# Kernel tuning notes

Measured on AMD Instinct MI355X. Metric: run time of the kernel, lower is better.

## Reference

```python
import jax, jax.numpy as jnp
import numpy as np

N = 50000        # nodes
E = 100000       # directed edges
F_NODE = 22      # atom features
F_EDGE = 4       # bond features
H = 64           # hidden_dim
EPS = 1e-5       # BatchNorm eps


def setup_inputs() -> dict:
    key = jax.random.key(0)
    ks = jax.random.split(key, 16)
    s = 0.05
    return {
        "x": jax.random.normal(ks[0], (N, F_NODE), dtype=jnp.float32),
        "edge_attr": jax.random.normal(ks[1], (E, F_EDGE), dtype=jnp.float32),
        "We1": jax.random.normal(ks[2], (F_EDGE, F_NODE * H), dtype=jnp.float32) * s,
        "be1": jnp.zeros((F_NODE * H,), dtype=jnp.float32),
        "root1": jax.random.normal(ks[3], (F_NODE, H), dtype=jnp.float32) * s,
        "b1": jnp.zeros((H,), dtype=jnp.float32),
        "g1": jnp.ones((H,), dtype=jnp.float32),
        "beta1": jnp.zeros((H,), dtype=jnp.float32),
        "We2": jax.random.normal(ks[4], (F_EDGE, H * H), dtype=jnp.float32) * s,
        "be2": jnp.zeros((H * H,), dtype=jnp.float32),
        "root2": jax.random.normal(ks[5], (H, H), dtype=jnp.float32) * s,
        "b2": jnp.zeros((H,), dtype=jnp.float32),
        "g2": jnp.ones((H,), dtype=jnp.float32),
        "beta2": jnp.zeros((H,), dtype=jnp.float32),
        "Wfc": jax.random.normal(ks[6], (H, 1), dtype=jnp.float32) * s,
        "bfc": jnp.zeros((1,), dtype=jnp.float32),
        "edge_index": jax.random.randint(ks[7], (2, E), 0, N, dtype=jnp.int32),
    }


def nnconv(x, edge_index, edge_attr, We, be, root, bias, in_ch, out_ch):
    # PyG NNConv (aggr='add', root_weight=True):
    #   out_i = x_i @ root + bias + sum_{(j->i)} x_j @ reshape(MLP(e_ji), [in, out])
    src, dst = edge_index[0], edge_index[1]
    w = jax.nn.relu(edge_attr @ We + be).reshape(-1, in_ch, out_ch)  # [E, in, out]
    msg = jnp.einsum('ei,eio->eo', x[src], w)                        # [E, out]
    agg = jax.ops.segment_sum(msg, dst, num_segments=x.shape[0])     # [N, out]
    return agg + x @ root + bias


def batchnorm(x, gamma, beta):
    # training-mode BatchNorm1d: batch statistics, biased variance
    mu = jnp.mean(x, axis=0)
    var = jnp.mean(jnp.square(x - mu), axis=0)
    return (x - mu) * jax.lax.rsqrt(var + EPS) * gamma + beta


def reference(x, edge_attr, We1, be1, root1, b1, g1, beta1,
              We2, be2, root2, b2, g2, beta2, Wfc, bfc, edge_index):
    h = nnconv(x, edge_index, edge_attr, We1, be1, root1, b1, F_NODE, H)
    h = jax.nn.relu(batchnorm(h, g1, beta1))
    # dropout is identity in eval / deterministic reference
    h = nnconv(h, edge_index, edge_attr, We2, be2, root2, b2, H, H)
    h = jax.nn.relu(batchnorm(h, g2, beta2))
    return jax.nn.sigmoid(h @ Wfc + bfc)  # [N, 1]
```

## Files before the change

### kernel.cpp

```cpp
#include <hip/hip_runtime.h>
#include <math.h>

#define N_NODES 50000
#define N_EDGES 100000
#define FNODE 22
#define HDIM 64
#define BN_EPS 1e-5f

typedef __attribute__((ext_vector_type(8))) short bfrag;
typedef __attribute__((ext_vector_type(4))) float facc;
typedef __attribute__((ext_vector_type(4))) unsigned int uint4v;

__device__ __forceinline__ unsigned f2bf(float x) {
    unsigned u = __float_as_uint(x);
    return (u + 0x7FFFu + ((u >> 16) & 1u)) >> 16;
}
__device__ __forceinline__ unsigned pk2bf(float lo, float hi) {
    return f2bf(lo) | (f2bf(hi) << 16);
}

template <int K>
__global__ void k_packB(const float* __restrict__ W, uint4v* __restrict__ Bt) {
    constexpr int NQ = (K + 31) / 32;
    int t = threadIdx.x;
    int ot = t >> 6, lane = t & 63;
    int o = ot * 16 + (lane & 15);
    int kg = lane >> 4;
#pragma unroll
    for (int q = 0; q < NQ; ++q) {
        unsigned w[4];
#pragma unroll
        for (int p = 0; p < 4; ++p) {
            int k0 = q * 32 + kg * 8 + 2 * p;
            float lo = (k0 < K) ? W[k0 * HDIM + o] : 0.f;
            float hi = (k0 + 1 < K) ? W[(k0 + 1) * HDIM + o] : 0.f;
            w[p] = pk2bf(lo, hi);
        }
        Bt[(ot * NQ + q) * 64 + lane] = uint4v{w[0], w[1], w[2], w[3]};
    }
}

__global__ void k_node1(const float* __restrict__ x, const uint4v* __restrict__ Bt1,
                        const float* __restrict__ b1, float* __restrict__ h1) {
    int lane = threadIdx.x & 63;
    int m = lane & 15, kg = lane >> 4, orow4 = kg * 4;
    int tile = blockIdx.x * 4 + (threadIdx.x >> 6);
    int nb = tile * 16;
    if (nb >= N_NODES) return;
    const float* xr = x + (size_t)(nb + m) * FNODE;
    float xv[8];
#pragma unroll
    for (int p = 0; p < 4; ++p) {
        int c = kg * 8 + 2 * p;
        float2 v = (c + 1 < FNODE) ? *(const float2*)(xr + c) : float2{0.f, 0.f};
        xv[2 * p] = v.x; xv[2 * p + 1] = v.y;
    }
    bfrag A = __builtin_bit_cast(bfrag, uint4v{pk2bf(xv[0], xv[1]), pk2bf(xv[2], xv[3]),
                                               pk2bf(xv[4], xv[5]), pk2bf(xv[6], xv[7])});
    const facc zero4 = {0.f, 0.f, 0.f, 0.f};
#pragma unroll
    for (int ot = 0; ot < 4; ++ot) {
        bfrag B = __builtin_bit_cast(bfrag, Bt1[ot * 64 + lane]);
        facc d = __builtin_amdgcn_mfma_f32_16x16x32_bf16(A, B, zero4, 0, 0, 0);
        float bv = b1[ot * 16 + m];
#pragma unroll
        for (int j = 0; j < 4; ++j)
            h1[(size_t)(nb + orow4 + j) * HDIM + ot * 16 + m] = d[j] + bv;
    }
}

template <int IN, int CHUNK>
__launch_bounds__(256, 6)
__global__ void k_edge(const float* __restrict__ h, const float* __restrict__ ea,
                       const float* __restrict__ We, const float* __restrict__ be,
                       const int* __restrict__ eidx, float* __restrict__ out) {
    constexpr int INH = IN * HDIM;
    constexpr int IP = IN / 2;
    __shared__ uint4v Wd[IP * 32];
    __shared__ unsigned Bp[IP * 32];

    int obeg = (blockIdx.x & 1) * 32;
    int tileblk = blockIdx.x >> 1;

    for (int idx = threadIdx.x; idx < IP * 32; idx += 256) {
        int ip = idx >> 5, oloc = idx & 31;
        int c0 = (2 * ip) * HDIM + obeg + oloc;
        int c1 = c0 + HDIM;
        Wd[idx] = uint4v{pk2bf(We[c0], We[INH + c0]),
                         pk2bf(We[2 * INH + c0], We[3 * INH + c0]),
                         pk2bf(We[c1], We[INH + c1]),
                         pk2bf(We[2 * INH + c1], We[3 * INH + c1])};
        Bp[idx] = pk2bf(be[c0], be[c1]);
    }
    __syncthreads();

    int lane = threadIdx.x & 63;
    int e16 = lane & 15;
    int orow4 = (lane >> 4) * 4;
    int tile = tileblk * 4 + (threadIdx.x >> 6);
    int ebase = tile * 16;
    if (ebase >= N_EDGES) return;

    bool act = lane < 16;
    float4 ea0 = ((const float4*)ea)[ebase + e16];
    bfrag A0 = __builtin_bit_cast(bfrag, uint4v{act ? pk2bf(ea0.x, ea0.y) : 0u,
                                                act ? pk2bf(ea0.z, ea0.w) : 0u, 0u, 0u});

    const char* hb = (const char*)h;
    unsigned offA[4];
#pragma unroll
    for (int j = 0; j < 4; ++j)
        offA[j] = (unsigned)eidx[ebase + orow4 + j] * (IN * 4);

    const facc zero4 = {0.f, 0.f, 0.f, 0.f};
    facc m0[2] = {zero4, zero4};

#pragma unroll
    for (int i0 = 0; i0 < IN; i0 += CHUNK) {
        float cA[4][CHUNK];
#pragma unroll
        for (int j = 0; j < 4; ++j) {
            if constexpr (CHUNK == 4) {
                float4 v = *(const float4*)(hb + offA[j] + (size_t)i0 * 4);
                cA[j][0] = v.x; cA[j][1] = v.y; cA[j][2] = v.z; cA[j][3] = v.w;
            } else {
                float2 v = *(const float2*)(hb + offA[j] + (size_t)i0 * 4);
                cA[j][0] = v.x; cA[j][1] = v.y;
            }
        }
#pragma unroll
        for (int t = 0; t < 2; ++t) {
#pragma unroll
            for (int d2 = 0; d2 < CHUNK / 2; ++d2) {
                int ip = i0 / 2 + d2;
                uint4v wq = Wd[ip * 32 + t * 16 + e16];
                unsigned bq = Bp[ip * 32 + t * 16 + e16];
                float bl = __uint_as_float(bq << 16);
                float bh = __uint_as_float(bq & 0xFFFF0000u);
                facc cl = {bl, bl, bl, bl};
                facc ch = {bh, bh, bh, bh};
                bfrag Blo = __builtin_bit_cast(bfrag, uint4v{wq.x, wq.y, 0u, 0u});
                bfrag Bhi = __builtin_bit_cast(bfrag, uint4v{wq.z, wq.w, 0u, 0u});
                facc t0 = __builtin_amdgcn_mfma_f32_16x16x32_bf16(A0, Blo, cl, 0, 0, 0);
#pragma unroll
                for (int j = 0; j < 4; ++j)
                    m0[t][j] = fmaf(cA[j][2 * d2], fmaxf(t0[j], 0.f), m0[t][j]);
                t0 = __builtin_amdgcn_mfma_f32_16x16x32_bf16(A0, Bhi, ch, 0, 0, 0);
#pragma unroll
                for (int j = 0; j < 4; ++j)
                    m0[t][j] = fmaf(cA[j][2 * d2 + 1], fmaxf(t0[j], 0.f), m0[t][j]);
            }
        }
    }

    int dA[4];
#pragma unroll
    for (int j = 0; j < 4; ++j)
        dA[j] = eidx[N_EDGES + ebase + orow4 + j];
#pragma unroll
    for (int t = 0; t < 2; ++t) {
#pragma unroll
        for (int j = 0; j < 4; ++j)
            atomicAdd(&out[(size_t)dA[j] * HDIM + obeg + t * 16 + e16], m0[t][j]);
    }
}

__global__ void k_stats(const float* __restrict__ hbuf, float* stats) {
    int c = threadIdx.x & 63;
    int r = threadIdx.x >> 6;
    int rowsPer = blockDim.x >> 6;
    float s = 0.f, q = 0.f;
    for (int n = blockIdx.x * rowsPer + r; n < N_NODES; n += gridDim.x * rowsPer) {
        float v = hbuf[n * HDIM + c];
        s += v;
        q = fmaf(v, v, q);
    }
    __shared__ float ls[4][64], lq[4][64];
    ls[r][c] = s;
    lq[r][c] = q;
    __syncthreads();
    if (r == 0) {
        s = ls[0][c] + ls[1][c] + ls[2][c] + ls[3][c];
        q = lq[0][c] + lq[1][c] + lq[2][c] + lq[3][c];
        atomicAdd(&stats[c], s);
        atomicAdd(&stats[64 + c], q);
    }
}

__global__ void k_finalize(const float* stats_in, const float* __restrict__ g,
                           const float* __restrict__ beta, float* as_out) {
    int c = threadIdx.x;
    float mu = stats_in[c] * (1.f / N_NODES);
    float var = stats_in[64 + c] * (1.f / N_NODES) - mu * mu;
    var = fmaxf(var, 0.f);
    float a = g[c] * rsqrtf(var + BN_EPS);
    as_out[c] = a;
    as_out[64 + c] = beta[c] - mu * a;
}

__global__ void k_apply1(const float* h1, const float* __restrict__ as1,
                         const uint4v* __restrict__ Bt, const float* __restrict__ b2,
                         float* __restrict__ h1n, float* h2) {
    int lane = threadIdx.x & 63;
    int m = lane & 15, kg = lane >> 4, orow4 = (lane >> 4) * 4;
    int tile = blockIdx.x * 4 + (threadIdx.x >> 6);
    int nb = tile * 16;
    if (nb >= N_NODES) return;
    int node = nb + m;
    const float* hr = h1 + (size_t)node * HDIM;

    float4 a0 = *(const float4*)(as1 + kg * 8), a1 = *(const float4*)(as1 + kg * 8 + 4);
    float4 s0 = *(const float4*)(as1 + 64 + kg * 8), s1 = *(const float4*)(as1 + 64 + kg * 8 + 4);
    float4 a2 = *(const float4*)(as1 + 32 + kg * 8), a3 = *(const float4*)(as1 + 32 + kg * 8 + 4);
    float4 s2 = *(const float4*)(as1 + 96 + kg * 8), s3 = *(const float4*)(as1 + 96 + kg * 8 + 4);

    float4 v0 = *(const float4*)(hr + kg * 8), v1 = *(const float4*)(hr + kg * 8 + 4);
    float4 v2 = *(const float4*)(hr + 32 + kg * 8), v3 = *(const float4*)(hr + 32 + kg * 8 + 4);

    float r0[8], r1[8];
#pragma unroll
    for (int p = 0; p < 4; ++p) {
        r0[p]     = fmaxf(fmaf((&v0.x)[p], (&a0.x)[p], (&s0.x)[p]), 0.f);
        r0[p + 4] = fmaxf(fmaf((&v1.x)[p], (&a1.x)[p], (&s1.x)[p]), 0.f);
        r1[p]     = fmaxf(fmaf((&v2.x)[p], (&a2.x)[p], (&s2.x)[p]), 0.f);
        r1[p + 4] = fmaxf(fmaf((&v3.x)[p], (&a3.x)[p], (&s3.x)[p]), 0.f);
    }
    *(float4*)(h1n + (size_t)node * HDIM + kg * 8)     = float4{r0[0], r0[1], r0[2], r0[3]};
    *(float4*)(h1n + (size_t)node * HDIM + kg * 8 + 4) = float4{r0[4], r0[5], r0[6], r0[7]};
    *(float4*)(h1n + (size_t)node * HDIM + 32 + kg * 8)     = float4{r1[0], r1[1], r1[2], r1[3]};
    *(float4*)(h1n + (size_t)node * HDIM + 32 + kg * 8 + 4) = float4{r1[4], r1[5], r1[6], r1[7]};

    bfrag A0 = __builtin_bit_cast(bfrag, uint4v{pk2bf(r0[0], r0[1]), pk2bf(r0[2], r0[3]),
                                                pk2bf(r0[4], r0[5]), pk2bf(r0[6], r0[7])});
    bfrag A1 = __builtin_bit_cast(bfrag, uint4v{pk2bf(r1[0], r1[1]), pk2bf(r1[2], r1[3]),
                                                pk2bf(r1[4], r1[5]), pk2bf(r1[6], r1[7])});

    const facc zero4 = {0.f, 0.f, 0.f, 0.f};
#pragma unroll
    for (int ot = 0; ot < 4; ++ot) {
        bfrag B0 = __builtin_bit_cast(bfrag, Bt[(ot * 2 + 0) * 64 + lane]);
        bfrag B1 = __builtin_bit_cast(bfrag, Bt[(ot * 2 + 1) * 64 + lane]);
        facc d = __builtin_amdgcn_mfma_f32_16x16x32_bf16(A0, B0, zero4, 0, 0, 0);
        d = __builtin_amdgcn_mfma_f32_16x16x32_bf16(A1, B1, d, 0, 0, 0);
        float bv = b2[ot * 16 + m];
#pragma unroll
        for (int j = 0; j < 4; ++j)
            h2[(size_t)(nb + orow4 + j) * HDIM + ot * 16 + m] = d[j] + bv;
    }
}

__global__ void k_final(const float* __restrict__ h2, const float* __restrict__ as2,
                        const float* __restrict__ Wfc, const float* __restrict__ bfc,
                        float* __restrict__ out) {
    int lane = threadIdx.x & 63;
    int n = blockIdx.x * (blockDim.x >> 6) + (threadIdx.x >> 6);
    if (n >= N_NODES) return;
    float a = as2[lane], s = as2[64 + lane];
    float v = fmaxf(fmaf(h2[n * HDIM + lane], a, s), 0.f) * Wfc[lane];
#pragma unroll
    for (int off = 32; off > 0; off >>= 1) v += __shfl_xor(v, off, 64);
    if (lane == 0) out[n] = 1.f / (1.f + expf(-(v + bfc[0])));
}

extern "C" void kernel_launch(void* const* d_in, const int* in_sizes, int n_in,
                              void* d_out, int out_size, void* d_ws, size_t ws_size,
                              hipStream_t stream) {
    const float* x     = (const float*)d_in[0];
    const float* ea    = (const float*)d_in[1];
    const float* We1   = (const float*)d_in[2];
    const float* be1   = (const float*)d_in[3];
    const float* root1 = (const float*)d_in[4];
    const float* b1    = (const float*)d_in[5];
    const float* g1    = (const float*)d_in[6];
    const float* beta1 = (const float*)d_in[7];
    const float* We2   = (const float*)d_in[8];
    const float* be2   = (const float*)d_in[9];
    const float* root2 = (const float*)d_in[10];
    const float* b2    = (const float*)d_in[11];
    const float* g2    = (const float*)d_in[12];
    const float* beta2 = (const float*)d_in[13];
    const float* Wfc   = (const float*)d_in[14];
    const float* bfc   = (const float*)d_in[15];
    const int*   eidx  = (const int*)d_in[16];
    float* out = (float*)d_out;

    char* ws = (char*)d_ws;
    const size_t nbuf = (size_t)N_NODES * HDIM * sizeof(float);
    float* h1    = (float*)ws;
    float* h1n   = (float*)(ws + nbuf);
    float* h2    = h1;
    float* stats = (float*)(ws + 2 * nbuf);
    uint4v* Bt2  = (uint4v*)(ws + 2 * nbuf + 4096);
    uint4v* Bt1  = (uint4v*)(ws + 2 * nbuf + 4096 + 8192);

    hipMemsetAsync(stats, 0, 512 * sizeof(float), stream);
    k_packB<HDIM><<<1, 256, 0, stream>>>(root2, Bt2);
    k_packB<FNODE><<<1, 256, 0, stream>>>(root1, Bt1);

    const int edgeBlocks = 2 * ((N_EDGES / 16 + 3) / 4);
    const int nodeBlocks = (N_NODES + 3) / 4;
    const int tileBlocks = (N_NODES / 16 + 3) / 4;

    k_node1<<<tileBlocks, 256, 0, stream>>>(x, Bt1, b1, h1);
    k_edge<FNODE, 2><<<edgeBlocks, 256, 0, stream>>>(x, ea, We1, be1, eidx, h1);
    k_stats<<<256, 256, 0, stream>>>(h1, stats);
    k_finalize<<<1, 64, 0, stream>>>(stats, g1, beta1, stats + 128);
    k_apply1<<<tileBlocks, 256, 0, stream>>>(h1, stats + 128, Bt2, b2, h1n, h2);
    k_edge<HDIM, 4><<<edgeBlocks, 256, 0, stream>>>(h1n, ea, We2, be2, eidx, h2);
    k_stats<<<256, 256, 0, stream>>>(h2, stats + 256);
    k_finalize<<<1, 64, 0, stream>>>(stats + 256, g2, beta2, stats + 384);
    k_final<<<nodeBlocks, 256, 0, stream>>>(h2, stats + 384, Wfc, bfc, out);
}
```

Before: 172.8 us.

## Replace atomic scatter-add with CSR-based gather reduction of per-edge messages

Builds a CSR index of edges grouped by destination node each call (count, scan, scatter kernels). Edge kernels now write per-edge messages to a buffer instead of doing float atomicAdds into node rows, and a new reduce kernel sums each node's incoming messages. This removes atomic contention. In exchange it adds a 25.6MB message buffer write and read per layer, plus several extra launches, including a single-block scan.

New measurement: 312.3 us. 80.8% more time.

```diff
diff --git a/kernel.cpp b/kernel.cpp
--- a/kernel.cpp
+++ b/kernel.cpp
@@ -17,6 +17,60 @@
 }
 __device__ __forceinline__ unsigned pk2bf(float lo, float hi) {
     return f2bf(lo) | (f2bf(hi) << 16);
+}
+
+__global__ void k_count(const int* __restrict__ eidx, int* __restrict__ cnt) {
+    int e = blockIdx.x * 256 + threadIdx.x;
+    if (e < N_EDGES) atomicAdd(&cnt[eidx[N_EDGES + e]], 1);
+}
+
+__global__ void k_scan(const int* __restrict__ cnt, int* __restrict__ base,
+                       int* __restrict__ cursor) {
+    __shared__ int part[1024];
+    int t = threadIdx.x;
+    const int PER = (N_NODES + 1023) / 1024;
+    int beg = t * PER;
+    int end = min(beg + PER, N_NODES);
+    int s = 0;
+    for (int i = beg; i < end; ++i) s += cnt[i];
+    part[t] = s;
+    __syncthreads();
+    for (int off = 1; off < 1024; off <<= 1) {
+        int v = part[t];
+        int u = (t >= off) ? part[t - off] : 0;
+        __syncthreads();
+        part[t] = v + u;
+        __syncthreads();
+    }
+    int run = (t == 0) ? 0 : part[t - 1];
+    for (int i = beg; i < end; ++i) {
+        base[i] = run;
+        cursor[i] = run;
+        run += cnt[i];
+    }
+    if (t == 1023) base[N_NODES] = part[1023];
+}
+
+__global__ void k_scatter(const int* __restrict__ eidx, int* __restrict__ cursor,
+                          int* __restrict__ csr) {
+    int e = blockIdx.x * 256 + threadIdx.x;
+    if (e < N_EDGES) {
+        int p = atomicAdd(&cursor[eidx[N_EDGES + e]], 1);
+        csr[p] = e;
+    }
+}
+
+__global__ void k_reduce(const float* __restrict__ basebuf, const float* __restrict__ msg,
+                         const int* __restrict__ base, const int* __restrict__ csr,
+                         float* __restrict__ hout) {
+    int lane = threadIdx.x & 63;
+    int n = blockIdx.x * 4 + (threadIdx.x >> 6);
+    if (n >= N_NODES) return;
+    float acc = basebuf[(size_t)n * HDIM + lane];
+    int b = base[n], e = base[n + 1];
+    for (int k = b; k < e; ++k)
+        acc += msg[(size_t)csr[k] * HDIM + lane];
+    hout[(size_t)n * HDIM + lane] = acc;
 }
 
 template <int K>
@@ -73,7 +127,7 @@
 __launch_bounds__(256, 6)
 __global__ void k_edge(const float* __restrict__ h, const float* __restrict__ ea,
                        const float* __restrict__ We, const float* __restrict__ be,
-                       const int* __restrict__ eidx, float* __restrict__ out) {
+                       const int* __restrict__ eidx, float* __restrict__ msg) {
     constexpr int INH = IN * HDIM;
     constexpr int IP = IN / 2;
     __shared__ uint4v Wd[IP * 32];
@@ -153,15 +207,11 @@
         }
     }
 
-    int dA[4];
-#pragma unroll
-    for (int j = 0; j < 4; ++j)
-        dA[j] = eidx[N_EDGES + ebase + orow4 + j];
 #pragma unroll
     for (int t = 0; t < 2; ++t) {
 #pragma unroll
         for (int j = 0; j < 4; ++j)
-            atomicAdd(&out[(size_t)dA[j] * HDIM + obeg + t * 16 + e16], m0[t][j]);
+            msg[(size_t)(ebase + orow4 + j) * HDIM + obeg + t * 16 + e16] = m0[t][j];
     }
 }
 
@@ -285,15 +335,27 @@
     float* out = (float*)d_out;
 
     char* ws = (char*)d_ws;
-    const size_t nbuf = (size_t)N_NODES * HDIM * sizeof(float);
+    const size_t nbuf  = (size_t)N_NODES * HDIM * sizeof(float);
+    const size_t msgsz = (size_t)N_EDGES * HDIM * sizeof(float);
     float* h1    = (float*)ws;
     float* h1n   = (float*)(ws + nbuf);
-    float* h2    = h1;
-    float* stats = (float*)(ws + 2 * nbuf);
-    uint4v* Bt2  = (uint4v*)(ws + 2 * nbuf + 4096);
-    uint4v* Bt1  = (uint4v*)(ws + 2 * nbuf + 4096 + 8192);
+    float* msg   = (float*)(ws + 2 * nbuf);
+    char*  meta  = ws + 2 * nbuf + msgsz;
+    float* stats = (float*)meta;
+    uint4v* Bt2  = (uint4v*)(meta + 2048);
+    uint4v* Bt1  = (uint4v*)(meta + 2048 + 8192);
+    int* cnt     = (int*)(meta + 16384);
+    int* cursor  = cnt + N_NODES;
+    int* base    = cursor + N_NODES;
+    int* csr     = base + N_NODES + 1;
 
     hipMemsetAsync(stats, 0, 512 * sizeof(float), stream);
+    hipMemsetAsync(cnt, 0, N_NODES * sizeof(int), stream);
+
+    const int eThreads = (N_EDGES + 255) / 256;
+    k_count<<<eThreads, 256, 0, stream>>>(eidx, cnt);
+    k_scan<<<1, 1024, 0, stream>>>(cnt, base, cursor);
+    k_scatter<<<eThreads, 256, 0, stream>>>(eidx, cursor, csr);
     k_packB<HDIM><<<1, 256, 0, stream>>>(root2, Bt2);
     k_packB<FNODE><<<1, 256, 0, stream>>>(root1, Bt1);
 
@@ -302,12 +364,14 @@
     const int tileBlocks = (N_NODES / 16 + 3) / 4;
 
     k_node1<<<tileBlocks, 256, 0, stream>>>(x, Bt1, b1, h1);
-    k_edge<FNODE, 2><<<edgeBlocks, 256, 0, stream>>>(x, ea, We1, be1, eidx, h1);
+    k_edge<FNODE, 2><<<edgeBlocks, 256, 0, stream>>>(x, ea, We1, be1, eidx, msg);
+    k_reduce<<<nodeBlocks, 256, 0, stream>>>(h1, msg, base, csr, h1);
     k_stats<<<256, 256, 0, stream>>>(h1, stats);
     k_finalize<<<1, 64, 0, stream>>>(stats, g1, beta1, stats + 128);
-    k_apply1<<<tileBlocks, 256, 0, stream>>>(h1, stats + 128, Bt2, b2, h1n, h2);
-    k_edge<HDIM, 4><<<edgeBlocks, 256, 0, stream>>>(h1n, ea, We2, be2, eidx, h2);
-    k_stats<<<256, 256, 0, stream>>>(h2, stats + 256);
+    k_apply1<<<tileBlocks, 256, 0, stream>>>(h1, stats + 128, Bt2, b2, h1n, h1);
+    k_edge<HDIM, 4><<<edgeBlocks, 256, 0, stream>>>(h1n, ea, We2, be2, eidx, msg);
+    k_reduce<<<nodeBlocks, 256, 0, stream>>>(h1, msg, base, csr, h1);
+    k_stats<<<256, 256, 0, stream>>>(h1, stats + 256);
     k_finalize<<<1, 64, 0, stream>>>(stats + 256, g2, beta2, stats + 384);
-    k_final<<<nodeBlocks, 256, 0, stream>>>(h2, stats + 384, Wfc, bfc, out);
-}
+    k_final<<<nodeBlocks, 256, 0, stream>>>(h1, stats + 384, Wfc, bfc, out);
+}
```

## Sort edges by destination and store gathered node features in bf16

Applied to the files above, without the earlier changes.

Adds a counting sort of edges by destination (count, three-stage scan, scatter), done every call, that also packs edge attributes to bf16. The edge kernels then gather bf16 source rows, halving gather bytes. Messages are summed per destination run through an LDS slab, and atomics are used only for runs that cross tile boundaries. This cuts atomic traffic and gather bandwidth, but adds several small preprocessing kernels with launch overhead and lowers occupancy to 4 blocks per CU.

Result: slower. 210.5 us (+21.8%).

```diff
diff --git a/kernel.cpp b/kernel.cpp
--- a/kernel.cpp
+++ b/kernel.cpp
@@ -10,6 +10,7 @@
 typedef __attribute__((ext_vector_type(8))) short bfrag;
 typedef __attribute__((ext_vector_type(4))) float facc;
 typedef __attribute__((ext_vector_type(4))) unsigned int uint4v;
+typedef __attribute__((ext_vector_type(2))) unsigned int uint2v;
 
 __device__ __forceinline__ unsigned f2bf(float x) {
     unsigned u = __float_as_uint(x);
@@ -17,6 +18,78 @@
 }
 __device__ __forceinline__ unsigned pk2bf(float lo, float hi) {
     return f2bf(lo) | (f2bf(hi) << 16);
+}
+__device__ __forceinline__ float bflo(unsigned w) { return __uint_as_float(w << 16); }
+__device__ __forceinline__ float bfhi(unsigned w) { return __uint_as_float(w & 0xFFFF0000u); }
+
+__global__ void k_count(const int* __restrict__ eidx, int* __restrict__ cnt) {
+    int e = blockIdx.x * 256 + threadIdx.x;
+    if (e < N_EDGES) atomicAdd(&cnt[eidx[N_EDGES + e]], 1);
+}
+
+__global__ void k_scanA(const int* __restrict__ cnt, int* __restrict__ excl,
+                        int* __restrict__ bsum) {
+    __shared__ int sh[256];
+    int g = blockIdx.x * 256 + threadIdx.x;
+    int c = (g < N_NODES) ? cnt[g] : 0;
+    sh[threadIdx.x] = c;
+    __syncthreads();
+    for (int off = 1; off < 256; off <<= 1) {
+        int v = sh[threadIdx.x];
+        int u = (threadIdx.x >= off) ? sh[threadIdx.x - off] : 0;
+        __syncthreads();
+        sh[threadIdx.x] = v + u;
+        __syncthreads();
+    }
+    if (g < N_NODES) excl[g] = sh[threadIdx.x] - c;
+    if (threadIdx.x == 255) bsum[blockIdx.x] = sh[255];
+}
+
+__global__ void k_scanB(const int* __restrict__ bsum, int* __restrict__ bbase, int nb) {
+    __shared__ int sh[256];
+    int t = threadIdx.x;
+    int v = (t < nb) ? bsum[t] : 0;
+    sh[t] = v;
+    __syncthreads();
+    for (int off = 1; off < 256; off <<= 1) {
+        int a = sh[t];
+        int u = (t >= off) ? sh[t - off] : 0;
+        __syncthreads();
+        sh[t] = a + u;
+        __syncthreads();
+    }
+    if (t < nb) bbase[t] = sh[t] - v;
+}
+
+__global__ void k_scanC(const int* __restrict__ excl, const int* __restrict__ bbase,
+                        int* __restrict__ cursor) {
+    int g = blockIdx.x * 256 + threadIdx.x;
+    if (g < N_NODES) cursor[g] = excl[g] + bbase[blockIdx.x];
+}
+
+__global__ void k_scatter(const int* __restrict__ eidx, const float* __restrict__ ea,
+                          int* __restrict__ cursor, int* __restrict__ srcsort,
+                          int* __restrict__ dstsort, uint2v* __restrict__ easort) {
+    int e = blockIdx.x * 256 + threadIdx.x;
+    if (e < N_EDGES) {
+        int d = eidx[N_EDGES + e];
+        int p = atomicAdd(&cursor[d], 1);
+        srcsort[p] = eidx[e];
+        dstsort[p] = d;
+        float4 v = ((const float4*)ea)[e];
+        easort[p] = uint2v{pk2bf(v.x, v.y), pk2bf(v.z, v.w)};
+    }
+}
+
+__global__ void k_packX(const float* __restrict__ x, unsigned* __restrict__ xbf) {
+    int idx = blockIdx.x * 256 + threadIdx.x;
+    if (idx < N_NODES * 12) {
+        int n = idx / 12, c2 = idx - n * 12;
+        int c = c2 * 2;
+        float lo = (c < FNODE) ? x[n * FNODE + c] : 0.f;
+        float hi = (c + 1 < FNODE) ? x[n * FNODE + c + 1] : 0.f;
+        xbf[idx] = pk2bf(lo, hi);
+    }
 }
 
 template <int K>
@@ -69,15 +142,17 @@
     }
 }
 
-template <int IN, int CHUNK>
-__launch_bounds__(256, 6)
-__global__ void k_edge(const float* __restrict__ h, const float* __restrict__ ea,
+template <int IN, int CHUNK, int ROWB>
+__launch_bounds__(256, 4)
+__global__ void k_edge(const char* __restrict__ hrows, const uint2v* __restrict__ easort,
+                       const int* __restrict__ srcsort, const int* __restrict__ dstsort,
                        const float* __restrict__ We, const float* __restrict__ be,
-                       const int* __restrict__ eidx, float* __restrict__ out) {
+                       float* __restrict__ out) {
     constexpr int INH = IN * HDIM;
     constexpr int IP = IN / 2;
     __shared__ uint4v Wd[IP * 32];
     __shared__ unsigned Bp[IP * 32];
+    __shared__ float slab[4][16 * 33];
 
     int obeg = (blockIdx.x & 1) * 32;
     int tileblk = blockIdx.x >> 1;
@@ -98,19 +173,18 @@
     int e16 = lane & 15;
     int orow4 = (lane >> 4) * 4;
     int tile = tileblk * 4 + (threadIdx.x >> 6);
-    int ebase = tile * 16;
-    if (ebase >= N_EDGES) return;
+    int s = tile * 16;
+    if (s >= N_EDGES) return;
+    float* sl = &slab[threadIdx.x >> 6][0];
 
     bool act = lane < 16;
-    float4 ea0 = ((const float4*)ea)[ebase + e16];
-    bfrag A0 = __builtin_bit_cast(bfrag, uint4v{act ? pk2bf(ea0.x, ea0.y) : 0u,
-                                                act ? pk2bf(ea0.z, ea0.w) : 0u, 0u, 0u});
-
-    const char* hb = (const char*)h;
+    uint2v eav = easort[s + e16];
+    bfrag A0 = __builtin_bit_cast(bfrag, uint4v{act ? eav.x : 0u, act ? eav.y : 0u, 0u, 0u});
+
     unsigned offA[4];
 #pragma unroll
     for (int j = 0; j < 4; ++j)
-        offA[j] = (unsigned)eidx[ebase + orow4 + j] * (IN * 4);
+        offA[j] = (unsigned)srcsort[s + orow4 + j] * ROWB;
 
     const facc zero4 = {0.f, 0.f, 0.f, 0.f};
     facc m0[2] = {zero4, zero4};
@@ -121,11 +195,12 @@
 #pragma unroll
         for (int j = 0; j < 4; ++j) {
             if constexpr (CHUNK == 4) {
-                float4 v = *(const float4*)(hb + offA[j] + (size_t)i0 * 4);
-                cA[j][0] = v.x; cA[j][1] = v.y; cA[j][2] = v.z; cA[j][3] = v.w;
+                uint2v hv = *(const uint2v*)(hrows + offA[j] + (size_t)i0 * 2);
+                cA[j][0] = bflo(hv.x); cA[j][1] = bfhi(hv.x);
+                cA[j][2] = bflo(hv.y); cA[j][3] = bfhi(hv.y);
             } else {
-                float2 v = *(const float2*)(hb + offA[j] + (size_t)i0 * 4);
-                cA[j][0] = v.x; cA[j][1] = v.y;
+                unsigned hv = *(const unsigned*)(hrows + offA[j] + (size_t)i0 * 2);
+                cA[j][0] = bflo(hv); cA[j][1] = bfhi(hv);
             }
         }
 #pragma unroll
@@ -135,8 +210,7 @@
                 int ip = i0 / 2 + d2;
                 uint4v wq = Wd[ip * 32 + t * 16 + e16];
                 unsigned bq = Bp[ip * 32 + t * 16 + e16];
-                float bl = __uint_as_float(bq << 16);
-                float bh = __uint_as_float(bq & 0xFFFF0000u);
+                float bl = bflo(bq), bh = bfhi(bq);
                 facc cl = {bl, bl, bl, bl};
                 facc ch = {bh, bh, bh, bh};
                 bfrag Blo = __builtin_bit_cast(bfrag, uint4v{wq.x, wq.y, 0u, 0u});
@@ -153,15 +227,34 @@
         }
     }
 
-    int dA[4];
-#pragma unroll
-    for (int j = 0; j < 4; ++j)
-        dA[j] = eidx[N_EDGES + ebase + orow4 + j];
-#pragma unroll
-    for (int t = 0; t < 2; ++t) {
+#pragma unroll
+    for (int t = 0; t < 2; ++t)
 #pragma unroll
         for (int j = 0; j < 4; ++j)
-            atomicAdd(&out[(size_t)dA[j] * HDIM + obeg + t * 16 + e16], m0[t][j]);
+            sl[(orow4 + j) * 33 + t * 16 + e16] = m0[t][j];
+
+    int dprev = (s > 0) ? dstsort[s - 1] : -1;
+    int dnext = (s + 16 < N_EDGES) ? dstsort[s + 16] : -1;
+    int col = lane & 31;
+    bool wlo = lane < 32;
+    float acc = 0.f;
+    int dcur = dstsort[s];
+    int runstart = 0;
+    for (int k = 0; k < 16; ++k) {
+        acc += sl[k * 33 + col];
+        bool isLast = (k == 15);
+        int dn = isLast ? -2 : dstsort[s + k + 1];
+        if (isLast || dn != dcur) {
+            bool unsafe = (runstart == 0 && dcur == dprev) || (isLast && dcur == dnext);
+            if (wlo) {
+                size_t idx = (size_t)dcur * HDIM + obeg + col;
+                if (unsafe) atomicAdd(&out[idx], acc);
+                else        out[idx] += acc;
+            }
+            acc = 0.f;
+            dcur = dn;
+            runstart = k + 1;
+        }
     }
 }
 
@@ -200,7 +293,7 @@
 
 __global__ void k_apply1(const float* h1, const float* __restrict__ as1,
                          const uint4v* __restrict__ Bt, const float* __restrict__ b2,
-                         float* __restrict__ h1n, float* h2) {
+                         unsigned* __restrict__ hbf, float* h2) {
     int lane = threadIdx.x & 63;
     int m = lane & 15, kg = lane >> 4, orow4 = (lane >> 4) * 4;
     int tile = blockIdx.x * 4 + (threadIdx.x >> 6);
@@ -225,15 +318,15 @@
         r1[p]     = fmaxf(fmaf((&v2.x)[p], (&a2.x)[p], (&s2.x)[p]), 0.f);
         r1[p + 4] = fmaxf(fmaf((&v3.x)[p], (&a3.x)[p], (&s3.x)[p]), 0.f);
     }
-    *(float4*)(h1n + (size_t)node * HDIM + kg * 8)     = float4{r0[0], r0[1], r0[2], r0[3]};
-    *(float4*)(h1n + (size_t)node * HDIM + kg * 8 + 4) = float4{r0[4], r0[5], r0[6], r0[7]};
-    *(float4*)(h1n + (size_t)node * HDIM + 32 + kg * 8)     = float4{r1[0], r1[1], r1[2], r1[3]};
-    *(float4*)(h1n + (size_t)node * HDIM + 32 + kg * 8 + 4) = float4{r1[4], r1[5], r1[6], r1[7]};
-
-    bfrag A0 = __builtin_bit_cast(bfrag, uint4v{pk2bf(r0[0], r0[1]), pk2bf(r0[2], r0[3]),
-                                                pk2bf(r0[4], r0[5]), pk2bf(r0[6], r0[7])});
-    bfrag A1 = __builtin_bit_cast(bfrag, uint4v{pk2bf(r1[0], r1[1]), pk2bf(r1[2], r1[3]),
-                                                pk2bf(r1[4], r1[5]), pk2bf(r1[6], r1[7])});
+    uint4v pk0 = uint4v{pk2bf(r0[0], r0[1]), pk2bf(r0[2], r0[3]),
+                        pk2bf(r0[4], r0[5]), pk2bf(r0[6], r0[7])};
+    uint4v pk1 = uint4v{pk2bf(r1[0], r1[1]), pk2bf(r1[2], r1[3]),
+                        pk2bf(r1[4], r1[5]), pk2bf(r1[6], r1[7])};
+    *(uint4v*)(hbf + (size_t)node * 32 + kg * 4)      = pk0;
+    *(uint4v*)(hbf + (size_t)node * 32 + 16 + kg * 4) = pk1;
+
+    bfrag A0 = __builtin_bit_cast(bfrag, pk0);
+    bfrag A1 = __builtin_bit_cast(bfrag, pk1);
 
     const facc zero4 = {0.f, 0.f, 0.f, 0.f};
 #pragma unroll
@@ -285,15 +378,34 @@
     float* out = (float*)d_out;
 
     char* ws = (char*)d_ws;
-    const size_t nbuf = (size_t)N_NODES * HDIM * sizeof(float);
-    float* h1    = (float*)ws;
-    float* h1n   = (float*)(ws + nbuf);
-    float* h2    = h1;
-    float* stats = (float*)(ws + 2 * nbuf);
-    uint4v* Bt2  = (uint4v*)(ws + 2 * nbuf + 4096);
-    uint4v* Bt1  = (uint4v*)(ws + 2 * nbuf + 4096 + 8192);
+    size_t off = 0;
+    auto alloc = [&](size_t bytes) { char* p = ws + off; off = (off + bytes + 255) & ~(size_t)255; return p; };
+    float*    h1      = (float*)alloc((size_t)N_NODES * HDIM * 4);
+    unsigned* hbf     = (unsigned*)alloc((size_t)N_NODES * 32 * 4);
+    unsigned* xbf     = (unsigned*)alloc((size_t)N_NODES * 12 * 4);
+    uint2v*   easort  = (uint2v*)alloc((size_t)N_EDGES * 8);
+    int*      srcsort = (int*)alloc((size_t)N_EDGES * 4);
+    int*      dstsort = (int*)alloc((size_t)N_EDGES * 4);
+    int*      cnt     = (int*)alloc((size_t)N_NODES * 4);
+    int*      cursor  = (int*)alloc((size_t)N_NODES * 4);
+    int*      excl    = (int*)alloc((size_t)N_NODES * 4);
+    int*      bsum    = (int*)alloc(256 * 4);
+    int*      bbase   = (int*)alloc(256 * 4);
+    float*    stats   = (float*)alloc(512 * 4);
+    uint4v*   Bt2     = (uint4v*)alloc(8 * 64 * 16);
+    uint4v*   Bt1     = (uint4v*)alloc(4 * 64 * 16);
 
     hipMemsetAsync(stats, 0, 512 * sizeof(float), stream);
+    hipMemsetAsync(cnt, 0, N_NODES * sizeof(int), stream);
+
+    const int eBlocks = (N_EDGES + 255) / 256;
+    const int nScanBlocks = (N_NODES + 255) / 256;
+    k_count<<<eBlocks, 256, 0, stream>>>(eidx, cnt);
+    k_scanA<<<nScanBlocks, 256, 0, stream>>>(cnt, excl, bsum);
+    k_scanB<<<1, 256, 0, stream>>>(bsum, bbase, nScanBlocks);
+    k_scanC<<<nScanBlocks, 256, 0, stream>>>(excl, bbase, cursor);
+    k_scatter<<<eBlocks, 256, 0, stream>>>(eidx, ea, cursor, srcsort, dstsort, easort);
+    k_packX<<<(N_NODES * 12 + 255) / 256, 256, 0, stream>>>(x, xbf);
     k_packB<HDIM><<<1, 256, 0, stream>>>(root2, Bt2);
     k_packB<FNODE><<<1, 256, 0, stream>>>(root1, Bt1);
 
@@ -302,12 +414,14 @@
     const int tileBlocks = (N_NODES / 16 + 3) / 4;
 
     k_node1<<<tileBlocks, 256, 0, stream>>>(x, Bt1, b1, h1);
-    k_edge<FNODE, 2><<<edgeBlocks, 256, 0, stream>>>(x, ea, We1, be1, eidx, h1);
+    k_edge<FNODE, 2, 48><<<edgeBlocks, 256, 0, stream>>>((const char*)xbf, easort, srcsort,
+                                                         dstsort, We1, be1, h1);
     k_stats<<<256, 256, 0, stream>>>(h1, stats);
     k_finalize<<<1, 64, 0, stream>>>(stats, g1, beta1, stats + 128);
-    k_apply1<<<tileBlocks, 256, 0, stream>>>(h1, stats + 128, Bt2, b2, h1n, h2);
-    k_edge<HDIM, 4><<<edgeBlocks, 256, 0, stream>>>(h1n, ea, We2, be2, eidx, h2);
-    k_stats<<<256, 256, 0, stream>>>(h2, stats + 256);
+    k_apply1<<<tileBlocks, 256, 0, stream>>>(h1, stats + 128, Bt2, b2, hbf, h1);
+    k_edge<HDIM, 4, 128><<<edgeBlocks, 256, 0, stream>>>((const char*)hbf, easort, srcsort,
+                                                         dstsort, We2, be2, h1);
+    k_stats<<<256, 256, 0, stream>>>(h1, stats + 256);
     k_finalize<<<1, 64, 0, stream>>>(stats + 256, g2, beta2, stats + 384);
-    k_final<<<nodeBlocks, 256, 0, stream>>>(h2, stats + 384, Wfc, bfc, out);
-}
+    k_final<<<nodeBlocks, 256, 0, stream>>>(h1, stats + 384, Wfc, bfc, out);
+}
```

## Gather bf16 source rows into LDS and fold edge bias into MFMA

Applied to the files above, without the earlier changes.

The edge kernel now gathers source node features as packed bf16 rows through cooperative coalesced loads into shared memory, instead of per-lane fp32 gathers from global memory. Layer 1 gets a new bf16 packing kernel for x, and apply1 writes a bf16 copy of the normalized hidden state in place of the fp32 one. The edge bias is moved into the MFMA as an extra K-column with a constant-one A entry, so each input channel takes one MFMA with a zero accumulator. This halves gather bandwidth and drops the bias broadcast, at the cost of an extra pack kernel, LDS staging, lower occupancy bounds and bf16 rounding of the gathered features.

Result: faster. 166.0 us, median of 2 (-3.9%).

```diff
diff --git a/kernel.cpp b/kernel.cpp
--- a/kernel.cpp
+++ b/kernel.cpp
@@ -17,6 +17,19 @@
 }
 __device__ __forceinline__ unsigned pk2bf(float lo, float hi) {
     return f2bf(lo) | (f2bf(hi) << 16);
+}
+__device__ __forceinline__ float bflo(unsigned w) { return __uint_as_float(w << 16); }
+__device__ __forceinline__ float bfhi(unsigned w) { return __uint_as_float(w & 0xFFFF0000u); }
+
+__global__ void k_packX(const float* __restrict__ x, unsigned* __restrict__ xbf) {
+    int idx = blockIdx.x * 256 + threadIdx.x;
+    if (idx < N_NODES * 12) {
+        int n = idx / 12, c2 = idx - n * 12;
+        int c = c2 * 2;
+        float lo = (c < FNODE) ? x[n * FNODE + c] : 0.f;
+        float hi = (c + 1 < FNODE) ? x[n * FNODE + c + 1] : 0.f;
+        xbf[idx] = pk2bf(lo, hi);
+    }
 }
 
 template <int K>
@@ -69,28 +82,24 @@
     }
 }
 
-template <int IN, int CHUNK>
-__launch_bounds__(256, 6)
-__global__ void k_edge(const float* __restrict__ h, const float* __restrict__ ea,
+template <int IN, int ROWB, int SSTRIDE, int MINW>
+__launch_bounds__(256, MINW)
+__global__ void k_edge(const char* __restrict__ hrows, const float* __restrict__ ea,
                        const float* __restrict__ We, const float* __restrict__ be,
                        const int* __restrict__ eidx, float* __restrict__ out) {
     constexpr int INH = IN * HDIM;
-    constexpr int IP = IN / 2;
-    __shared__ uint4v Wd[IP * 32];
-    __shared__ unsigned Bp[IP * 32];
+    __shared__ uint4v Wf[IN * 32];
+    __shared__ float hsl[4][16 * SSTRIDE];
 
     int obeg = (blockIdx.x & 1) * 32;
     int tileblk = blockIdx.x >> 1;
 
-    for (int idx = threadIdx.x; idx < IP * 32; idx += 256) {
-        int ip = idx >> 5, oloc = idx & 31;
-        int c0 = (2 * ip) * HDIM + obeg + oloc;
-        int c1 = c0 + HDIM;
-        Wd[idx] = uint4v{pk2bf(We[c0], We[INH + c0]),
-                         pk2bf(We[2 * INH + c0], We[3 * INH + c0]),
-                         pk2bf(We[c1], We[INH + c1]),
-                         pk2bf(We[2 * INH + c1], We[3 * INH + c1])};
-        Bp[idx] = pk2bf(be[c0], be[c1]);
+    for (int idx = threadIdx.x; idx < IN * 32; idx += 256) {
+        int i = idx >> 5, oloc = idx & 31;
+        int c = i * HDIM + obeg + oloc;
+        Wf[idx] = uint4v{pk2bf(We[c], We[INH + c]),
+                         pk2bf(We[2 * INH + c], We[3 * INH + c]),
+                         f2bf(be[c]), 0u};
     }
     __syncthreads();
 
@@ -100,55 +109,66 @@
     int tile = tileblk * 4 + (threadIdx.x >> 6);
     int ebase = tile * 16;
     if (ebase >= N_EDGES) return;
+    float* hs = &hsl[threadIdx.x >> 6][0];
 
     bool act = lane < 16;
     float4 ea0 = ((const float4*)ea)[ebase + e16];
+    unsigned aone = act ? 0x3F80u : 0u;
     bfrag A0 = __builtin_bit_cast(bfrag, uint4v{act ? pk2bf(ea0.x, ea0.y) : 0u,
-                                                act ? pk2bf(ea0.z, ea0.w) : 0u, 0u, 0u});
-
-    const char* hb = (const char*)h;
-    unsigned offA[4];
-#pragma unroll
-    for (int j = 0; j < 4; ++j)
-        offA[j] = (unsigned)eidx[ebase + orow4 + j] * (IN * 4);
+                                                act ? pk2bf(ea0.z, ea0.w) : 0u, aone, 0u});
+
+    constexpr int SLOTS = 16 * (ROWB / 16);
+    constexpr int SPR = ROWB / 16;
+#pragma unroll
+    for (int p = 0; p < (SLOTS + 63) / 64; ++p) {
+        int idx = p * 64 + lane;
+        if ((SLOTS % 64 == 0) || idx < SLOTS) {
+            int r = idx / SPR, c16 = idx - r * SPR;
+            int src = eidx[ebase + r];
+            uint4v hv = *(const uint4v*)(hrows + (size_t)src * ROWB + c16 * 16);
+            *(float4*)&hs[r * SSTRIDE + c16 * 8] =
+                float4{bflo(hv.x), bfhi(hv.x), bflo(hv.y), bfhi(hv.y)};
+            *(float4*)&hs[r * SSTRIDE + c16 * 8 + 4] =
+                float4{bflo(hv.z), bfhi(hv.z), bflo(hv.w), bfhi(hv.w)};
+        }
+    }
 
     const facc zero4 = {0.f, 0.f, 0.f, 0.f};
     facc m0[2] = {zero4, zero4};
 
-#pragma unroll
-    for (int i0 = 0; i0 < IN; i0 += CHUNK) {
-        float cA[4][CHUNK];
-#pragma unroll
-        for (int j = 0; j < 4; ++j) {
-            if constexpr (CHUNK == 4) {
-                float4 v = *(const float4*)(hb + offA[j] + (size_t)i0 * 4);
-                cA[j][0] = v.x; cA[j][1] = v.y; cA[j][2] = v.z; cA[j][3] = v.w;
-            } else {
-                float2 v = *(const float2*)(hb + offA[j] + (size_t)i0 * 4);
-                cA[j][0] = v.x; cA[j][1] = v.y;
+    constexpr int I4 = IN & ~3;
+#pragma unroll
+    for (int i0 = 0; i0 < I4; i0 += 4) {
+        float4 hA[4];
+#pragma unroll
+        for (int j = 0; j < 4; ++j)
+            hA[j] = *(const float4*)&hs[(orow4 + j) * SSTRIDE + i0];
+#pragma unroll
+        for (int di = 0; di < 4; ++di) {
+#pragma unroll
+            for (int t = 0; t < 2; ++t) {
+                bfrag B = __builtin_bit_cast(bfrag, Wf[(i0 + di) * 32 + t * 16 + e16]);
+                facc t0 = __builtin_amdgcn_mfma_f32_16x16x32_bf16(A0, B, zero4, 0, 0, 0);
+#pragma unroll
+                for (int j = 0; j < 4; ++j)
+                    m0[t][j] = fmaf((&hA[j].x)[di], fmaxf(t0[j], 0.f), m0[t][j]);
             }
         }
-#pragma unroll
-        for (int t = 0; t < 2; ++t) {
-#pragma unroll
-            for (int d2 = 0; d2 < CHUNK / 2; ++d2) {
-                int ip = i0 / 2 + d2;
-                uint4v wq = Wd[ip * 32 + t * 16 + e16];
-                unsigned bq = Bp[ip * 32 + t * 16 + e16];
-                float bl = __uint_as_float(bq << 16);
-                float bh = __uint_as_float(bq & 0xFFFF0000u);
-                facc cl = {bl, bl, bl, bl};
-                facc ch = {bh, bh, bh, bh};
-                bfrag Blo = __builtin_bit_cast(bfrag, uint4v{wq.x, wq.y, 0u, 0u});
-                bfrag Bhi = __builtin_bit_cast(bfrag, uint4v{wq.z, wq.w, 0u, 0u});
-                facc t0 = __builtin_amdgcn_mfma_f32_16x16x32_bf16(A0, Blo, cl, 0, 0, 0);
+    }
+    if constexpr ((IN & 3) != 0) {
+        float4 hA[4];
+#pragma unroll
+        for (int j = 0; j < 4; ++j)
+            hA[j] = *(const float4*)&hs[(orow4 + j) * SSTRIDE + I4];
+#pragma unroll
+        for (int di = 0; di < (IN & 3); ++di) {
+#pragma unroll
+            for (int t = 0; t < 2; ++t) {
+                bfrag B = __builtin_bit_cast(bfrag, Wf[(I4 + di) * 32 + t * 16 + e16]);
+                facc t0 = __builtin_amdgcn_mfma_f32_16x16x32_bf16(A0, B, zero4, 0, 0, 0);
 #pragma unroll
                 for (int j = 0; j < 4; ++j)
-                    m0[t][j] = fmaf(cA[j][2 * d2], fmaxf(t0[j], 0.f), m0[t][j]);
-                t0 = __builtin_amdgcn_mfma_f32_16x16x32_bf16(A0, Bhi, ch, 0, 0, 0);
-#pragma unroll
-                for (int j = 0; j < 4; ++j)
-                    m0[t][j] = fmaf(cA[j][2 * d2 + 1], fmaxf(t0[j], 0.f), m0[t][j]);
+                    m0[t][j] = fmaf((&hA[j].x)[di], fmaxf(t0[j], 0.f), m0[t][j]);
             }
         }
     }
@@ -200,7 +220,7 @@
 
 __global__ void k_apply1(const float* h1, const float* __restrict__ as1,
                          const uint4v* __restrict__ Bt, const float* __restrict__ b2,
-                         float* __restrict__ h1n, float* h2) {
+                         unsigned* __restrict__ hbf, float* h2) {
     int lane = threadIdx.x & 63;
     int m = lane & 15, kg = lane >> 4, orow4 = (lane >> 4) * 4;
     int tile = blockIdx.x * 4 + (threadIdx.x >> 6);
@@ -225,15 +245,15 @@
         r1[p]     = fmaxf(fmaf((&v2.x)[p], (&a2.x)[p], (&s2.x)[p]), 0.f);
         r1[p + 4] = fmaxf(fmaf((&v3.x)[p], (&a3.x)[p], (&s3.x)[p]), 0.f);
     }
-    *(float4*)(h1n + (size_t)node * HDIM + kg * 8)     = float4{r0[0], r0[1], r0[2], r0[3]};
-    *(float4*)(h1n + (size_t)node * HDIM + kg * 8 + 4) = float4{r0[4], r0[5], r0[6], r0[7]};
-    *(float4*)(h1n + (size_t)node * HDIM + 32 + kg * 8)     = float4{r1[0], r1[1], r1[2], r1[3]};
-    *(float4*)(h1n + (size_t)node * HDIM + 32 + kg * 8 + 4) = float4{r1[4], r1[5], r1[6], r1[7]};
-
-    bfrag A0 = __builtin_bit_cast(bfrag, uint4v{pk2bf(r0[0], r0[1]), pk2bf(r0[2], r0[3]),
-                                                pk2bf(r0[4], r0[5]), pk2bf(r0[6], r0[7])});
-    bfrag A1 = __builtin_bit_cast(bfrag, uint4v{pk2bf(r1[0], r1[1]), pk2bf(r1[2], r1[3]),
-                                                pk2bf(r1[4], r1[5]), pk2bf(r1[6], r1[7])});
+    uint4v pk0 = uint4v{pk2bf(r0[0], r0[1]), pk2bf(r0[2], r0[3]),
+                        pk2bf(r0[4], r0[5]), pk2bf(r0[6], r0[7])};
+    uint4v pk1 = uint4v{pk2bf(r1[0], r1[1]), pk2bf(r1[2], r1[3]),
+                        pk2bf(r1[4], r1[5]), pk2bf(r1[6], r1[7])};
+    *(uint4v*)(hbf + (size_t)node * 32 + kg * 4)      = pk0;
+    *(uint4v*)(hbf + (size_t)node * 32 + 16 + kg * 4) = pk1;
+
+    bfrag A0 = __builtin_bit_cast(bfrag, pk0);
+    bfrag A1 = __builtin_bit_cast(bfrag, pk1);
 
     const facc zero4 = {0.f, 0.f, 0.f, 0.f};
 #pragma unroll
@@ -285,15 +305,17 @@
     float* out = (float*)d_out;
 
     char* ws = (char*)d_ws;
-    const size_t nbuf = (size_t)N_NODES * HDIM * sizeof(float);
-    float* h1    = (float*)ws;
-    float* h1n   = (float*)(ws + nbuf);
-    float* h2    = h1;
-    float* stats = (float*)(ws + 2 * nbuf);
-    uint4v* Bt2  = (uint4v*)(ws + 2 * nbuf + 4096);
-    uint4v* Bt1  = (uint4v*)(ws + 2 * nbuf + 4096 + 8192);
+    size_t off = 0;
+    auto alloc = [&](size_t bytes) { char* p = ws + off; off = (off + bytes + 255) & ~(size_t)255; return p; };
+    float*    h1    = (float*)alloc((size_t)N_NODES * HDIM * 4);
+    unsigned* hbf   = (unsigned*)alloc((size_t)N_NODES * 32 * 4);
+    unsigned* xbf   = (unsigned*)alloc((size_t)N_NODES * 12 * 4);
+    float*    stats = (float*)alloc(512 * 4);
+    uint4v*   Bt2   = (uint4v*)alloc(8 * 64 * 16);
+    uint4v*   Bt1   = (uint4v*)alloc(4 * 64 * 16);
 
     hipMemsetAsync(stats, 0, 512 * sizeof(float), stream);
+    k_packX<<<(N_NODES * 12 + 255) / 256, 256, 0, stream>>>(x, xbf);
     k_packB<HDIM><<<1, 256, 0, stream>>>(root2, Bt2);
     k_packB<FNODE><<<1, 256, 0, stream>>>(root1, Bt1);
 
@@ -302,12 +324,14 @@
     const int tileBlocks = (N_NODES / 16 + 3) / 4;
 
     k_node1<<<tileBlocks, 256, 0, stream>>>(x, Bt1, b1, h1);
-    k_edge<FNODE, 2><<<edgeBlocks, 256, 0, stream>>>(x, ea, We1, be1, eidx, h1);
+    k_edge<FNODE, 48, 28, 4><<<edgeBlocks, 256, 0, stream>>>((const char*)xbf, ea,
+                                                             We1, be1, eidx, h1);
     k_stats<<<256, 256, 0, stream>>>(h1, stats);
     k_finalize<<<1, 64, 0, stream>>>(stats, g1, beta1, stats + 128);
-    k_apply1<<<tileBlocks, 256, 0, stream>>>(h1, stats + 128, Bt2, b2, h1n, h2);
-    k_edge<HDIM, 4><<<edgeBlocks, 256, 0, stream>>>(h1n, ea, We2, be2, eidx, h2);
-    k_stats<<<256, 256, 0, stream>>>(h2, stats + 256);
+    k_apply1<<<tileBlocks, 256, 0, stream>>>(h1, stats + 128, Bt2, b2, hbf, h1);
+    k_edge<HDIM, 128, 68, 3><<<edgeBlocks, 256, 0, stream>>>((const char*)hbf, ea,
+                                                             We2, be2, eidx, h1);
+    k_stats<<<256, 256, 0, stream>>>(h1, stats + 256);
     k_finalize<<<1, 64, 0, stream>>>(stats + 256, g2, beta2, stats + 384);
-    k_final<<<nodeBlocks, 256, 0, stream>>>(h2, stats + 384, Wfc, bfc, out);
-}
+    k_final<<<nodeBlocks, 256, 0, stream>>>(h1, stats + 384, Wfc, bfc, out);
+}
```
